# Kernel optimization log

Hardware: AMD Instinct MI355X
Metric: run time of the kernel (lower is better)

The kernel has to match this reference:

```python
import jax, jax.numpy as jnp
import numpy as np

B, N, C = 8, 4096, 768
H = 8            # num_heads (hardcoded in module)
D = C // H       # head_dim = 96


def setup_inputs() -> dict:
    key = jax.random.key(0)
    ks = jax.random.split(key, 10)
    s = 0.02
    return {
        "x_rgb": jax.random.normal(ks[0], (B, N, C), dtype=jnp.float32),
        "x_depth": jax.random.normal(ks[1], (B, N, C), dtype=jnp.float32),
        "W_qkv_rgb": jax.random.normal(ks[2], (3 * C, C), dtype=jnp.float32) * s,
        "b_qkv_rgb": jnp.zeros((3 * C,), dtype=jnp.float32),
        "W_qkv_depth": jax.random.normal(ks[3], (2 * C, C), dtype=jnp.float32) * s,
        "b_qkv_depth": jnp.zeros((2 * C,), dtype=jnp.float32),
        "W_out": jax.random.normal(ks[4], (C, C), dtype=jnp.float32) * s,
        "b_out": jnp.zeros((C,), dtype=jnp.float32),
        "adaptive_weights": jnp.ones((2,), dtype=jnp.float32),
    }


def reference(x_rgb, x_depth, W_qkv_rgb, b_qkv_rgb, W_qkv_depth, b_qkv_depth,
              W_out, b_out, adaptive_weights):
    scale = 1.0 / (D ** 0.5)
    # qkv projections (torch Linear: x @ W.T + b)
    qkv_rgb = (x_rgb @ W_qkv_rgb.T + b_qkv_rgb).reshape(B, N, 3, H, D)
    q_rgb, k_rgb, v_rgb = qkv_rgb[:, :, 0], qkv_rgb[:, :, 1], qkv_rgb[:, :, 2]
    kv_depth = (x_depth @ W_qkv_depth.T + b_qkv_depth).reshape(B, N, 2, H, D)
    k_depth, v_depth = kv_depth[:, :, 0], kv_depth[:, :, 1]

    # per-token attention across the head axis: scores are [B,N,H,H]
    attn_rgb = jax.nn.softmax(
        jnp.einsum('bnqd,bnkd->bnqk', q_rgb, k_depth) * scale, axis=-1)
    attn_depth = jax.nn.softmax(
        jnp.einsum('bnqd,bnkd->bnqk', q_rgb, k_rgb) * scale, axis=-1)

    # NOTE: faithful to original einsum with independent labels k and v:
    # sums over k (softmax -> 1) and over v independently.
    wv_rgb = jnp.einsum('bnqk,bnvd->bnqd', attn_rgb, v_depth)
    wv_depth = jnp.einsum('bnqk,bnvd->bnqd', attn_depth, v_rgb)

    w = jax.nn.sigmoid(adaptive_weights)
    x_fusion = (w[0] * wv_rgb + w[1] * wv_depth).reshape(B, N, C)
    x_fusion = x_fusion @ W_out.T + b_out
    return (x_rgb, x_fusion)
```

## Files before the change

kernel.cpp:

```cpp
#include <hip/hip_runtime.h>

typedef unsigned short u16;
typedef __attribute__((ext_vector_type(8))) short bf16x8;
typedef __attribute__((ext_vector_type(4))) float f32x4;

#define M_TOT 32768

__device__ __forceinline__ u16 f2b(float x) {
    union { float f; unsigned u; } c; c.f = x;
    unsigned r = c.u + 0x7fffu + ((c.u >> 16) & 1u);
    return (u16)(r >> 16);
}

#define BAR() do { __builtin_amdgcn_sched_barrier(0); \
                   __builtin_amdgcn_s_barrier(); \
                   __builtin_amdgcn_sched_barrier(0); } while (0)
#define LGKM0() asm volatile("s_waitcnt lgkmcnt(0)" ::: "memory")

__global__ void prep_b1(const float* __restrict__ Wr, const float* __restrict__ Wd,
                        const float* __restrict__ br, const float* __restrict__ bd,
                        const float* __restrict__ aw,
                        u16* __restrict__ B1, float* __restrict__ fb) {
    int id = blockIdx.x * 256 + threadIdx.x;
    if (id >= 96 * 1536) return;
    int d = id / 1536, k = id - d * 1536;
    float w0 = 1.f / (1.f + __expf(-aw[0]));
    float w1 = 1.f / (1.f + __expf(-aw[1]));
    float s = 0.f, v;
    if (k < 768) {
        for (int h = 0; h < 8; h++) s += Wr[(size_t)(1536 + h * 96 + d) * 768 + k];
        v = w1 * s;
    } else {
        for (int h = 0; h < 8; h++) s += Wd[(size_t)(768 + h * 96 + d) * 768 + (k - 768)];
        v = w0 * s;
    }
    B1[id] = f2b(v);
    if (k == 0) {
        float t = 0.f;
        for (int h = 0; h < 8; h++)
            t += w1 * br[1536 + h * 96 + d] + w0 * bd[768 + h * 96 + d];
        fb[d] = t;
    }
}

__global__ void prep_weff(const float* __restrict__ Wo, u16* __restrict__ Weff) {
    int id = blockIdx.x * 256 + threadIdx.x;
    if (id >= 768 * 96) return;
    int c = id / 96, d = id - c * 96;
    float s = 0.f;
    for (int h = 0; h < 8; h++) s += Wo[(size_t)c * 768 + h * 96 + d];
    Weff[id] = f2b(s);
}

#define LDF 72

__device__ __forceinline__ void stage_issue(const float* __restrict__ Xr,
                                            const float* __restrict__ Xd,
                                            const u16* __restrict__ B1,
                                            int m0, int tid, int n,
                                            float4 (&aF)[4], uint4 (&bF)[3]) {
    const float* __restrict__ X = (n < 12) ? Xr : Xd;
    const int kx = (n < 12) ? n * 64 : n * 64 - 768;
#pragma unroll
    for (int r = 0; r < 4; r++) {
        int c = tid + 256 * r, row = c >> 4, colc = (c & 15) * 4;
        aF[r] = *(const float4*)&X[(size_t)(m0 + row) * 768 + kx + colc];
    }
#pragma unroll
    for (int r = 0; r < 3; r++) {
        int c = tid + 256 * r, row = c >> 3, colc = (c & 7) * 8;
        bF[r] = *(const uint4*)&B1[(size_t)row * 1536 + n * 64 + colc];
    }
}

__device__ __forceinline__ void stage_commit(float* __restrict__ out0,
                                             int m0, int tid, int n,
                                             const float4 (&aF)[4], const uint4 (&bF)[3],
                                             u16* __restrict__ sAb, u16* __restrict__ sBb) {
#pragma unroll
    for (int r = 0; r < 4; r++) {
        int c = tid + 256 * r, row = c >> 4, colc = (c & 15) * 4;
        if (n < 12)
            *(float4*)&out0[(size_t)(m0 + row) * 768 + n * 64 + colc] = aF[r];
        ushort4 bv;
        bv.x = f2b(aF[r].x); bv.y = f2b(aF[r].y);
        bv.z = f2b(aF[r].z); bv.w = f2b(aF[r].w);
        *(ushort4*)&sAb[row * LDF + colc] = bv;
    }
#pragma unroll
    for (int r = 0; r < 3; r++) {
        int c = tid + 256 * r, row = c >> 3, colc = (c & 7) * 8;
        *(uint4*)&sBb[row * LDF + colc] = bF[r];
    }
}

__device__ __forceinline__ void mfma_tile(const u16* __restrict__ sAb,
                                          const u16* __restrict__ sBb,
                                          int wave, int fr, int fk, f32x4 (&acc)[6]) {
#pragma unroll
    for (int s = 0; s < 2; s++) {
        bf16x8 a = *(const bf16x8*)&sAb[(wave * 16 + fr) * LDF + s * 32 + fk];
#pragma unroll
        for (int j = 0; j < 6; j++) {
            bf16x8 b = *(const bf16x8*)&sBb[(j * 16 + fr) * LDF + s * 32 + fk];
            acc[j] = __builtin_amdgcn_mfma_f32_16x16x32_bf16(a, b, acc[j], 0, 0, 0);
        }
    }
}

__global__ __launch_bounds__(256) void gemm_f(const float* __restrict__ Xr,
                                              const float* __restrict__ Xd,
                                              const u16* __restrict__ B1,
                                              const float* __restrict__ fb,
                                              float* __restrict__ out0,
                                              u16* __restrict__ fbuf) {
    __shared__ u16 sA[2][64 * LDF];
    __shared__ u16 sB[2][96 * LDF];
    const int tid = threadIdx.x;
    const int m0 = blockIdx.x * 64;
    const int lane = tid & 63, wave = tid >> 6;
    const int fr = lane & 15, fk = (lane >> 4) * 8;

    f32x4 acc[6] = {};
    float4 a0[4], a1[4];
    uint4  b0[3], b1[3];

    stage_issue(Xr, Xd, B1, m0, tid, 0, a0, b0);
    stage_issue(Xr, Xd, B1, m0, tid, 1, a1, b1);
    stage_commit(out0, m0, tid, 0, a0, b0, &sA[0][0], &sB[0][0]);
    LGKM0(); BAR();

    for (int t = 0; t < 24; t += 2) {
        if (t + 2 < 24) stage_issue(Xr, Xd, B1, m0, tid, t + 2, a0, b0);
        mfma_tile(&sA[0][0], &sB[0][0], wave, fr, fk, acc);
        BAR();
        stage_commit(out0, m0, tid, t + 1, a1, b1, &sA[1][0], &sB[1][0]);
        LGKM0(); BAR();

        if (t + 3 < 24) stage_issue(Xr, Xd, B1, m0, tid, t + 3, a1, b1);
        mfma_tile(&sA[1][0], &sB[1][0], wave, fr, fk, acc);
        if (t + 2 < 24) {
            BAR();
            stage_commit(out0, m0, tid, t + 2, a0, b0, &sA[0][0], &sB[0][0]);
            LGKM0(); BAR();
        }
    }

    const int em = (lane >> 4) * 4, en = lane & 15;
#pragma unroll
    for (int j = 0; j < 6; j++) {
        int dcol = j * 16 + en;
        float bias = fb[dcol];
#pragma unroll
        for (int r = 0; r < 4; r++) {
            int row = m0 + wave * 16 + em + r;
            fbuf[(size_t)row * 96 + dcol] = f2b(acc[j][r] + bias);
        }
    }
}

__global__ __launch_bounds__(256) void gemm_o(const u16* __restrict__ fbuf,
                                              const u16* __restrict__ Weff,
                                              const float* __restrict__ bout,
                                              float* __restrict__ out1) {
    const int tid = threadIdx.x;
    const int lane = tid & 63;
    const int wv = (blockIdx.x << 2) | (tid >> 6);
    const int mg = wv >> 3;
    const int nc = (wv & 7) * 96;
    const int fr = lane & 15, fk = (lane >> 4) << 3;

    const u16* pa = fbuf + (size_t)((mg << 4) | fr) * 96 + fk;
    bf16x8 A0 = *(const bf16x8*)(pa);
    bf16x8 A1 = *(const bf16x8*)(pa + 32);
    bf16x8 A2 = *(const bf16x8*)(pa + 64);

    const u16* pb = Weff + (size_t)(nc + fr) * 96 + fk;
    f32x4 acc[6] = {};
#pragma unroll
    for (int j = 0; j < 6; j++) {
        const u16* pbj = pb + j * 1536;
        acc[j] = __builtin_amdgcn_mfma_f32_16x16x32_bf16(
            A0, *(const bf16x8*)(pbj), acc[j], 0, 0, 0);
        acc[j] = __builtin_amdgcn_mfma_f32_16x16x32_bf16(
            A1, *(const bf16x8*)(pbj + 32), acc[j], 0, 0, 0);
        acc[j] = __builtin_amdgcn_mfma_f32_16x16x32_bf16(
            A2, *(const bf16x8*)(pbj + 64), acc[j], 0, 0, 0);
    }

    const int em = (lane >> 4) << 2, en = lane & 15;
    const int orow = (mg << 4) + em;
#pragma unroll
    for (int j = 0; j < 6; j++) {
        const int col = nc + j * 16 + en;
        const float bias = bout[col];
#pragma unroll
        for (int r = 0; r < 4; r++)
            out1[(size_t)(orow + r) * 768 + col] = acc[j][r] + bias;
    }
}

extern "C" void kernel_launch(void* const* d_in, const int* in_sizes, int n_in,
                              void* d_out, int out_size, void* d_ws, size_t ws_size,
                              hipStream_t stream) {
    const float* x_rgb       = (const float*)d_in[0];
    const float* x_depth     = (const float*)d_in[1];
    const float* W_qkv_rgb   = (const float*)d_in[2];
    const float* b_qkv_rgb   = (const float*)d_in[3];
    const float* W_qkv_depth = (const float*)d_in[4];
    const float* b_qkv_depth = (const float*)d_in[5];
    const float* W_out       = (const float*)d_in[6];
    const float* b_out       = (const float*)d_in[7];
    const float* aw          = (const float*)d_in[8];

    float* out0 = (float*)d_out;
    float* out1 = out0 + (size_t)M_TOT * 768;

    char* w = (char*)d_ws;
    u16*   B1   = (u16*)w;
    float* fb   = (float*)(w + 294912);
    u16*   Weff = (u16*)(w + 294912 + 512);
    u16*   fbuf = (u16*)(w + 294912 + 512 + 147456);

    prep_b1<<<576, 256, 0, stream>>>(W_qkv_rgb, W_qkv_depth, b_qkv_rgb, b_qkv_depth,
                                     aw, B1, fb);
    prep_weff<<<288, 256, 0, stream>>>(W_out, Weff);
    gemm_f<<<512, 256, 0, stream>>>(x_rgb, x_depth, B1, fb, out0, fbuf);
    gemm_o<<<4096, 256, 0, stream>>>(fbuf, Weff, b_out, out1);
}
```

Measured before the change: 404.6 us.

## Merge prep kernels and move x_rgb passthrough copy into output GEMM launch

Result: slower. 424.9 us (+5.0%).

```diff
diff --git a/kernel.cpp b/kernel.cpp
--- a/kernel.cpp
+++ b/kernel.cpp
@@ -17,39 +17,40 @@
                    __builtin_amdgcn_sched_barrier(0); } while (0)
 #define LGKM0() asm volatile("s_waitcnt lgkmcnt(0)" ::: "memory")
 
-__global__ void prep_b1(const float* __restrict__ Wr, const float* __restrict__ Wd,
-                        const float* __restrict__ br, const float* __restrict__ bd,
-                        const float* __restrict__ aw,
-                        u16* __restrict__ B1, float* __restrict__ fb) {
-    int id = blockIdx.x * 256 + threadIdx.x;
-    if (id >= 96 * 1536) return;
-    int d = id / 1536, k = id - d * 1536;
-    float w0 = 1.f / (1.f + __expf(-aw[0]));
-    float w1 = 1.f / (1.f + __expf(-aw[1]));
-    float s = 0.f, v;
-    if (k < 768) {
-        for (int h = 0; h < 8; h++) s += Wr[(size_t)(1536 + h * 96 + d) * 768 + k];
-        v = w1 * s;
+__global__ void prep(const float* __restrict__ Wr, const float* __restrict__ Wd,
+                     const float* __restrict__ br, const float* __restrict__ bd,
+                     const float* __restrict__ aw, const float* __restrict__ Wo,
+                     u16* __restrict__ B1, float* __restrict__ fb,
+                     u16* __restrict__ Weff) {
+    if (blockIdx.x < 576) {
+        int id = blockIdx.x * 256 + threadIdx.x;
+        if (id >= 96 * 1536) return;
+        int d = id / 1536, k = id - d * 1536;
+        float w0 = 1.f / (1.f + __expf(-aw[0]));
+        float w1 = 1.f / (1.f + __expf(-aw[1]));
+        float s = 0.f, v;
+        if (k < 768) {
+            for (int h = 0; h < 8; h++) s += Wr[(size_t)(1536 + h * 96 + d) * 768 + k];
+            v = w1 * s;
+        } else {
+            for (int h = 0; h < 8; h++) s += Wd[(size_t)(768 + h * 96 + d) * 768 + (k - 768)];
+            v = w0 * s;
+        }
+        B1[id] = f2b(v);
+        if (k == 0) {
+            float t = 0.f;
+            for (int h = 0; h < 8; h++)
+                t += w1 * br[1536 + h * 96 + d] + w0 * bd[768 + h * 96 + d];
+            fb[d] = t;
+        }
     } else {
-        for (int h = 0; h < 8; h++) s += Wd[(size_t)(768 + h * 96 + d) * 768 + (k - 768)];
-        v = w0 * s;
-    }
-    B1[id] = f2b(v);
-    if (k == 0) {
-        float t = 0.f;
-        for (int h = 0; h < 8; h++)
-            t += w1 * br[1536 + h * 96 + d] + w0 * bd[768 + h * 96 + d];
-        fb[d] = t;
-    }
-}
-
-__global__ void prep_weff(const float* __restrict__ Wo, u16* __restrict__ Weff) {
-    int id = blockIdx.x * 256 + threadIdx.x;
-    if (id >= 768 * 96) return;
-    int c = id / 96, d = id - c * 96;
-    float s = 0.f;
-    for (int h = 0; h < 8; h++) s += Wo[(size_t)c * 768 + h * 96 + d];
-    Weff[id] = f2b(s);
+        int id = (blockIdx.x - 576) * 256 + threadIdx.x;
+        if (id >= 768 * 96) return;
+        int c = id / 96, d = id - c * 96;
+        float s = 0.f;
+        for (int h = 0; h < 8; h++) s += Wo[(size_t)c * 768 + h * 96 + d];
+        Weff[id] = f2b(s);
+    }
 }
 
 #define LDF 72
@@ -73,15 +74,12 @@
     }
 }
 
-__device__ __forceinline__ void stage_commit(float* __restrict__ out0,
-                                             int m0, int tid, int n,
+__device__ __forceinline__ void stage_commit(int tid,
                                              const float4 (&aF)[4], const uint4 (&bF)[3],
                                              u16* __restrict__ sAb, u16* __restrict__ sBb) {
 #pragma unroll
     for (int r = 0; r < 4; r++) {
         int c = tid + 256 * r, row = c >> 4, colc = (c & 15) * 4;
-        if (n < 12)
-            *(float4*)&out0[(size_t)(m0 + row) * 768 + n * 64 + colc] = aF[r];
         ushort4 bv;
         bv.x = f2b(aF[r].x); bv.y = f2b(aF[r].y);
         bv.z = f2b(aF[r].z); bv.w = f2b(aF[r].w);
@@ -112,7 +110,6 @@
                                               const float* __restrict__ Xd,
                                               const u16* __restrict__ B1,
                                               const float* __restrict__ fb,
-                                              float* __restrict__ out0,
                                               u16* __restrict__ fbuf) {
     __shared__ u16 sA[2][64 * LDF];
     __shared__ u16 sB[2][96 * LDF];
@@ -127,21 +124,21 @@
 
     stage_issue(Xr, Xd, B1, m0, tid, 0, a0, b0);
     stage_issue(Xr, Xd, B1, m0, tid, 1, a1, b1);
-    stage_commit(out0, m0, tid, 0, a0, b0, &sA[0][0], &sB[0][0]);
+    stage_commit(tid, a0, b0, &sA[0][0], &sB[0][0]);
     LGKM0(); BAR();
 
     for (int t = 0; t < 24; t += 2) {
         if (t + 2 < 24) stage_issue(Xr, Xd, B1, m0, tid, t + 2, a0, b0);
         mfma_tile(&sA[0][0], &sB[0][0], wave, fr, fk, acc);
         BAR();
-        stage_commit(out0, m0, tid, t + 1, a1, b1, &sA[1][0], &sB[1][0]);
+        stage_commit(tid, a1, b1, &sA[1][0], &sB[1][0]);
         LGKM0(); BAR();
 
         if (t + 3 < 24) stage_issue(Xr, Xd, B1, m0, tid, t + 3, a1, b1);
         mfma_tile(&sA[1][0], &sB[1][0], wave, fr, fk, acc);
         if (t + 2 < 24) {
             BAR();
-            stage_commit(out0, m0, tid, t + 2, a0, b0, &sA[0][0], &sB[0][0]);
+            stage_commit(tid, a0, b0, &sA[0][0], &sB[0][0]);
             LGKM0(); BAR();
         }
     }
@@ -159,11 +156,23 @@
     }
 }
 
-__global__ __launch_bounds__(256) void gemm_o(const u16* __restrict__ fbuf,
-                                              const u16* __restrict__ Weff,
-                                              const float* __restrict__ bout,
-                                              float* __restrict__ out1) {
+__global__ __launch_bounds__(256) void gemm_oc(const u16* __restrict__ fbuf,
+                                               const u16* __restrict__ Weff,
+                                               const float* __restrict__ bout,
+                                               const float* __restrict__ Xr,
+                                               float* __restrict__ out0,
+                                               float* __restrict__ out1) {
     const int tid = threadIdx.x;
+    if (blockIdx.x >= 4096) {
+        const size_t base = (size_t)(blockIdx.x - 4096) * 256 + tid;
+        const float4* __restrict__ src = (const float4*)Xr;
+        float4* __restrict__ dst = (float4*)out0;
+#pragma unroll
+        for (int q = 0; q < 12; q++)
+            dst[base + (size_t)q * 524288] = src[base + (size_t)q * 524288];
+        return;
+    }
+
     const int lane = tid & 63;
     const int wv = (blockIdx.x << 2) | (tid >> 6);
     const int mg = wv >> 3;
@@ -222,9 +231,8 @@
     u16*   Weff = (u16*)(w + 294912 + 512);
     u16*   fbuf = (u16*)(w + 294912 + 512 + 147456);
 
-    prep_b1<<<576, 256, 0, stream>>>(W_qkv_rgb, W_qkv_depth, b_qkv_rgb, b_qkv_depth,
-                                     aw, B1, fb);
-    prep_weff<<<288, 256, 0, stream>>>(W_out, Weff);
-    gemm_f<<<512, 256, 0, stream>>>(x_rgb, x_depth, B1, fb, out0, fbuf);
-    gemm_o<<<4096, 256, 0, stream>>>(fbuf, Weff, b_out, out1);
-}
+    prep<<<864, 256, 0, stream>>>(W_qkv_rgb, W_qkv_depth, b_qkv_rgb, b_qkv_depth,
+                                  aw, W_out, B1, fb, Weff);
+    gemm_f<<<512, 256, 0, stream>>>(x_rgb, x_depth, B1, fb, fbuf);
+    gemm_oc<<<6144, 256, 0, stream>>>(fbuf, Weff, b_out, x_rgb, out0, out1);
+}
```
